# Kernel optimization log

Measured on AMD Instinct MI355X. Metric: run time of the kernel, lower is better.

Reference implementation:

```python
import jax, jax.numpy as jnp
import numpy as np

EPS = 1e-5

def _face_normals(v, vi):
    # v: [B,V,3], vi: [F,3] -> [B,F,3]
    pts = v[:, vi]                                  # [B,F,3,3]
    n = jnp.cross(pts[:, :, 1] - pts[:, :, 0], pts[:, :, 2] - pts[:, :, 0])
    norm = jnp.linalg.norm(n, axis=-1, keepdims=True)
    return n / jnp.where(norm < EPS, 1.0, norm)

def _vert_normals(v, vi):
    fn = _face_normals(v, vi)                       # [B,F,3]
    fn_rep = jnp.repeat(fn, 3, axis=1)              # [B,3F,3] (one copy per face vertex)
    vn = jnp.zeros_like(v).at[:, vi.reshape(-1)].add(fn_rep)
    norm = jnp.linalg.norm(vn, axis=-1, keepdims=True)
    return vn / jnp.where(norm < EPS, 1.0, norm)

def _values_to_uv(values, index_image, bary_image):
    # values: [B,V,C]; index_image/bary_image: [U,U,3] -> [B,C,U,U]
    mask = jnp.all(index_image != -1, axis=-1)      # [U,U]
    idx = jnp.clip(index_image, 0, values.shape[1] - 1)
    vals = values[:, idx]                           # [B,U,U,3,C]
    uv = jnp.einsum('buvkc,uvk->bcuv', vals, bary_image.astype(values.dtype))
    return uv * mask[None, None].astype(values.dtype)

def _grid_sample_bilinear(img, gx, gy):
    # img: [B,C,H,W]; gx,gy: [N] in [-1,1]; align_corners=False, zero padding
    B, C, H, W = img.shape
    ix = ((gx + 1.0) * W - 1.0) * 0.5
    iy = ((gy + 1.0) * H - 1.0) * 0.5
    x0 = jnp.floor(ix); y0 = jnp.floor(iy)
    x1 = x0 + 1.0;      y1 = y0 + 1.0
    wx1 = ix - x0; wx0 = 1.0 - wx1
    wy1 = iy - y0; wy0 = 1.0 - wy1
    def gather(xi, yi):
        valid = (xi >= 0) & (xi < W) & (yi >= 0) & (yi < H)
        xc = jnp.clip(xi, 0, W - 1).astype(jnp.int32)
        yc = jnp.clip(yi, 0, H - 1).astype(jnp.int32)
        return img[:, :, yc, xc] * valid.astype(img.dtype)  # [B,C,N]
    return (gather(x0, y0) * (wx0 * wy0) + gather(x1, y0) * (wx1 * wy0)
          + gather(x0, y1) * (wx0 * wy1) + gather(x1, y1) * (wx1 * wy1))

def _sample_uv(values_uv, uv_coords, v2uv):
    g = uv_coords * 2.0 - 1.0                       # [T,2]
    vals = _grid_sample_bilinear(values_uv, g[:, 0], g[:, 1])  # [B,C,T]
    vals = jnp.transpose(vals, (0, 2, 1))           # [B,T,C]
    return vals[:, v2uv].mean(axis=2)               # [B,V,C]

def setup_inputs() -> dict:
    key = jax.random.key(0)
    ks = jax.random.split(key, 6)
    B, V, Fc, U, T, K = 8, 100000, 200000, 1024, 110000, 2
    verts = jax.random.normal(ks[0], (B, V, 3), jnp.float32)
    vi = jax.random.randint(ks[1], (Fc, 3), 0, V, dtype=jnp.int32)
    index_image = jax.random.randint(ks[2], (U, U, 3), 0, V, dtype=jnp.int32)
    bary_image = jax.random.uniform(ks[3], (U, U, 3), jnp.float32)
    vt = jax.random.uniform(ks[4], (T, 2), jnp.float32)
    v2uv = jax.random.randint(ks[5], (V, K), 0, T, dtype=jnp.int32)
    return {"verts": verts, "bary_image": bary_image, "vt": vt,
            "vi": vi, "index_image": index_image, "v2uv": v2uv}

def reference(verts, bary_image, vt, vi, index_image, v2uv):
    vn = _vert_normals(verts, vi)                   # [B,V,3]
    uv = _values_to_uv(vn, index_image, bary_image) # [B,3,U,U]
    return _sample_uv(uv, vt, v2uv)                 # [B,V,3]
```

## Files before the change

kernel.cpp:

```cpp
#include <hip/hip_runtime.h>

#define EPS 1e-5f

constexpr int B = 8;
constexpr int V = 100000;
constexpr int F = 200000;
constexpr int U = 1024;
constexpr int T = 110000;
constexpr int ELLCAP = 32;

constexpr int TRB = (V + 255) / 256;
constexpr int CZB = (V + 255) / 256;
constexpr int ELB = (3 * F + 255) / 256;
constexpr int FNB = (F * 8 + 255) / 256;
constexpr int CPB = (T + 255) / 256;

struct Corner { int i0, i1, i2; float w0, w1, w2; };

__global__ void k1_pre(const float* __restrict__ verts,
                       float4* __restrict__ vertsT,
                       int* __restrict__ cnt) {
    int blk = blockIdx.x;
    if (blk < TRB) {
        int v = blk * 256 + threadIdx.x;
        if (v >= V) return;
        float4 row[8];
#pragma unroll
        for (int b = 0; b < 8; ++b) {
            const float* p = verts + (size_t)b * V * 3 + (size_t)v * 3;
            row[b] = make_float4(p[0], p[1], p[2], 0.0f);
        }
        float4* dst = vertsT + (size_t)v * 8;
#pragma unroll
        for (int b = 0; b < 8; ++b) dst[b] = row[b];
    } else {
        int i = (blk - TRB) * 256 + threadIdx.x;
        if (i < V) cnt[i] = 0;
    }
}

__global__ void k2_fused(const int* __restrict__ vi,
                         int* __restrict__ cnt,
                         int* __restrict__ ell,
                         const float4* __restrict__ vertsT,
                         float4* __restrict__ fn,
                         const int* __restrict__ index_image,
                         const float* __restrict__ bary_image,
                         const float* __restrict__ vt,
                         Corner* __restrict__ corners) {
    int blk = blockIdx.x;

    if (blk < ELB) {
        int e = blk * 256 + threadIdx.x;
        if (e >= 3 * F) return;
        int v = vi[e];
        int pos = atomicAdd(&cnt[v], 1);
        if (pos < ELLCAP) ell[v * ELLCAP + pos] = e / 3;
        return;
    }

    if (blk < ELB + FNB) {
        int id = (blk - ELB) * 256 + threadIdx.x;
        if (id >= F * 8) return;
        int f = id >> 3;
        int b = id & 7;

        int i0 = vi[f * 3 + 0];
        int i1 = vi[f * 3 + 1];
        int i2 = vi[f * 3 + 2];

        float4 p0 = vertsT[(size_t)i0 * 8 + b];
        float4 p1 = vertsT[(size_t)i1 * 8 + b];
        float4 p2 = vertsT[(size_t)i2 * 8 + b];

        float e1x = p1.x - p0.x, e1y = p1.y - p0.y, e1z = p1.z - p0.z;
        float e2x = p2.x - p0.x, e2y = p2.y - p0.y, e2z = p2.z - p0.z;

        float nx = e1y * e2z - e1z * e2y;
        float ny = e1z * e2x - e1x * e2z;
        float nz = e1x * e2y - e1y * e2x;

        float norm = sqrtf(nx * nx + ny * ny + nz * nz);
        float inv = (norm < EPS) ? 1.0f : (1.0f / norm);
        fn[id] = make_float4(nx * inv, ny * inv, nz * inv, 0.0f);
        return;
    }

    int t = (blk - ELB - FNB) * 256 + threadIdx.x;
    if (t >= T) return;

    float gx = vt[t * 2 + 0];
    float gy = vt[t * 2 + 1];
    float ix = gx * (float)U - 0.5f;
    float iy = gy * (float)U - 0.5f;

    float x0f = floorf(ix);
    float y0f = floorf(iy);
    int x0 = (int)x0f;
    int y0 = (int)y0f;
    float wx1 = ix - x0f, wx0 = 1.0f - wx1;
    float wy1 = iy - y0f, wy0 = 1.0f - wy1;

#pragma unroll
    for (int c = 0; c < 4; ++c) {
        int cy = c >> 1, cx = c & 1;
        int y = y0 + cy;
        int x = x0 + cx;
        Corner cr;
        if (x >= 0 && x < U && y >= 0 && y < U) {
            float w = (cy ? wy1 : wy0) * (cx ? wx1 : wx0);
            int pix = y * U + x;
            int i0 = index_image[pix * 3 + 0];
            int i1 = index_image[pix * 3 + 1];
            int i2 = index_image[pix * 3 + 2];
            float m = (i0 != -1 && i1 != -1 && i2 != -1) ? 1.0f : 0.0f;
            float wm = w * m;
            cr.i0 = min(max(i0, 0), V - 1);
            cr.i1 = min(max(i1, 0), V - 1);
            cr.i2 = min(max(i2, 0), V - 1);
            cr.w0 = wm * bary_image[pix * 3 + 0];
            cr.w1 = wm * bary_image[pix * 3 + 1];
            cr.w2 = wm * bary_image[pix * 3 + 2];
        } else {
            cr.i0 = 0; cr.i1 = 0; cr.i2 = 0;
            cr.w0 = 0.0f; cr.w1 = 0.0f; cr.w2 = 0.0f;
        }
        corners[t * 4 + c] = cr;
    }
}

__global__ void gather_vn(const float4* __restrict__ fn,
                          const int* __restrict__ cnt,
                          const int* __restrict__ ell,
                          float4* __restrict__ vn) {
    int id = blockIdx.x * blockDim.x + threadIdx.x;
    if (id >= V * 8) return;
    int v = id >> 3;
    int b = id & 7;

    int deg = min(cnt[v], ELLCAP);
    const int* row = ell + (size_t)v * ELLCAP;

    float ax = 0.0f, ay = 0.0f, az = 0.0f;
    for (int j = 0; j < deg; ++j) {
        int f = row[j];
        float4 n = fn[(size_t)f * 8 + b];
        ax += n.x; ay += n.y; az += n.z;
    }

    float n = sqrtf(ax * ax + ay * ay + az * az);
    float inv = (n < EPS) ? 1.0f : (1.0f / n);
    vn[id] = make_float4(ax * inv, ay * inv, az * inv, 0.0f);
}

__global__ void sample_points(const float4* __restrict__ vn,
                              const Corner* __restrict__ corners,
                              float4* __restrict__ vals) {
    int id = blockIdx.x * blockDim.x + threadIdx.x;
    if (id >= T * 8) return;
    int t = id >> 3;
    int b = id & 7;

    float ax = 0.0f, ay = 0.0f, az = 0.0f;
#pragma unroll
    for (int c = 0; c < 4; ++c) {
        Corner cr = corners[t * 4 + c];
        float4 q0 = vn[(size_t)cr.i0 * 8 + b];
        float4 q1 = vn[(size_t)cr.i1 * 8 + b];
        float4 q2 = vn[(size_t)cr.i2 * 8 + b];
        ax += cr.w0 * q0.x + cr.w1 * q1.x + cr.w2 * q2.x;
        ay += cr.w0 * q0.y + cr.w1 * q1.y + cr.w2 * q2.y;
        az += cr.w0 * q0.z + cr.w1 * q1.z + cr.w2 * q2.z;
    }

    vals[id] = make_float4(ax, ay, az, 0.0f);
}

__global__ void gather_out(const float4* __restrict__ vals,
                           const int* __restrict__ v2uv,
                           float* __restrict__ out) {
    int id = blockIdx.x * blockDim.x + threadIdx.x;
    if (id >= V * 8) return;
    int v = id >> 3;
    int b = id & 7;

    int t0 = v2uv[v * 2 + 0];
    int t1 = v2uv[v * 2 + 1];
    float4 x = vals[(size_t)t0 * 8 + b];
    float4 y = vals[(size_t)t1 * 8 + b];

    float* o = out + (size_t)b * V * 3 + (size_t)v * 3;
    o[0] = 0.5f * (x.x + y.x);
    o[1] = 0.5f * (x.y + y.y);
    o[2] = 0.5f * (x.z + y.z);
}

extern "C" void kernel_launch(void* const* d_in, const int* in_sizes, int n_in,
                              void* d_out, int out_size, void* d_ws, size_t ws_size,
                              hipStream_t stream) {
    const float* verts   = (const float*)d_in[0];
    const float* bary    = (const float*)d_in[1];
    const float* vt      = (const float*)d_in[2];
    const int*   vi      = (const int*)d_in[3];
    const int*   idx_img = (const int*)d_in[4];
    const int*   v2uv    = (const int*)d_in[5];
    float* out = (float*)d_out;

    float4* vertsT  = (float4*)d_ws;
    float4* vn      = vertsT;
    float4* fn      = vertsT + (size_t)V * 8;
    float4* vals    = fn;
    int*    cnt     = (int*)(fn + (size_t)F * 8);
    int*    ell     = cnt + V;
    Corner* corners = (Corner*)(ell + (size_t)V * ELLCAP);

    const int BLK = 256;
    k1_pre<<<TRB + CZB, BLK, 0, stream>>>(verts, vertsT, cnt);
    k2_fused<<<ELB + FNB + CPB, BLK, 0, stream>>>(
        vi, cnt, ell, vertsT, fn, idx_img, bary, vt, corners);
    gather_vn<<<(V * 8 + BLK - 1) / BLK, BLK, 0, stream>>>(fn, cnt, ell, vn);
    sample_points<<<(T * 8 + BLK - 1) / BLK, BLK, 0, stream>>>(vn, corners, vals);
    gather_out<<<(V * 8 + BLK - 1) / BLK, BLK, 0, stream>>>(vals, v2uv, out);
}
```

Before: 208.0 us.

## Build per-block vertex adjacency in shared memory instead of global ELL atomics

Removes the global ELL adjacency build, which used atomics on a global count array plus a zeroing pass. Each 512-thread workgroup instead scans the full face-index array, collects the incident faces of its own 512 vertices into a shared-memory list with shared atomics, and then sums face normals for them. This drops the global atomics, the ELL table traffic and one zeroing pass. In exchange, every one of the ~196 workgroups rereads the entire index array (~2.4 MB), which greatly increases total read traffic. The per-vertex capacity also drops from 32 to 28.

```diff
diff --git a/kernel.cpp b/kernel.cpp
--- a/kernel.cpp
+++ b/kernel.cpp
@@ -7,41 +7,33 @@
 constexpr int F = 200000;
 constexpr int U = 1024;
 constexpr int T = 110000;
-constexpr int ELLCAP = 32;
 
 constexpr int TRB = (V + 255) / 256;
-constexpr int CZB = (V + 255) / 256;
-constexpr int ELB = (3 * F + 255) / 256;
 constexpr int FNB = (F * 8 + 255) / 256;
 constexpr int CPB = (T + 255) / 256;
 
+constexpr int VPW = 512;
+constexpr int KWG = (V + VPW - 1) / VPW;
+constexpr int CAP = 28;
+
 struct Corner { int i0, i1, i2; float w0, w1, w2; };
 
-__global__ void k1_pre(const float* __restrict__ verts,
-                       float4* __restrict__ vertsT,
-                       int* __restrict__ cnt) {
-    int blk = blockIdx.x;
-    if (blk < TRB) {
-        int v = blk * 256 + threadIdx.x;
-        if (v >= V) return;
-        float4 row[8];
-#pragma unroll
-        for (int b = 0; b < 8; ++b) {
-            const float* p = verts + (size_t)b * V * 3 + (size_t)v * 3;
-            row[b] = make_float4(p[0], p[1], p[2], 0.0f);
-        }
-        float4* dst = vertsT + (size_t)v * 8;
-#pragma unroll
-        for (int b = 0; b < 8; ++b) dst[b] = row[b];
-    } else {
-        int i = (blk - TRB) * 256 + threadIdx.x;
-        if (i < V) cnt[i] = 0;
-    }
+__global__ void k1_transpose(const float* __restrict__ verts,
+                             float4* __restrict__ vertsT) {
+    int v = blockIdx.x * blockDim.x + threadIdx.x;
+    if (v >= V) return;
+    float4 row[8];
+#pragma unroll
+    for (int b = 0; b < 8; ++b) {
+        const float* p = verts + (size_t)b * V * 3 + (size_t)v * 3;
+        row[b] = make_float4(p[0], p[1], p[2], 0.0f);
+    }
+    float4* dst = vertsT + (size_t)v * 8;
+#pragma unroll
+    for (int b = 0; b < 8; ++b) dst[b] = row[b];
 }
 
 __global__ void k2_fused(const int* __restrict__ vi,
-                         int* __restrict__ cnt,
-                         int* __restrict__ ell,
                          const float4* __restrict__ vertsT,
                          float4* __restrict__ fn,
                          const int* __restrict__ index_image,
@@ -50,17 +42,8 @@
                          Corner* __restrict__ corners) {
     int blk = blockIdx.x;
 
-    if (blk < ELB) {
-        int e = blk * 256 + threadIdx.x;
-        if (e >= 3 * F) return;
-        int v = vi[e];
-        int pos = atomicAdd(&cnt[v], 1);
-        if (pos < ELLCAP) ell[v * ELLCAP + pos] = e / 3;
-        return;
-    }
-
-    if (blk < ELB + FNB) {
-        int id = (blk - ELB) * 256 + threadIdx.x;
+    if (blk < FNB) {
+        int id = blk * 256 + threadIdx.x;
         if (id >= F * 8) return;
         int f = id >> 3;
         int b = id & 7;
@@ -86,7 +69,7 @@
         return;
     }
 
-    int t = (blk - ELB - FNB) * 256 + threadIdx.x;
+    int t = (blk - FNB) * 256 + threadIdx.x;
     if (t >= T) return;
 
     float gx = vt[t * 2 + 0];
@@ -129,28 +112,56 @@
     }
 }
 
-__global__ void gather_vn(const float4* __restrict__ fn,
-                          const int* __restrict__ cnt,
-                          const int* __restrict__ ell,
-                          float4* __restrict__ vn) {
-    int id = blockIdx.x * blockDim.x + threadIdx.x;
-    if (id >= V * 8) return;
-    int v = id >> 3;
-    int b = id & 7;
-
-    int deg = min(cnt[v], ELLCAP);
-    const int* row = ell + (size_t)v * ELLCAP;
-
-    float ax = 0.0f, ay = 0.0f, az = 0.0f;
-    for (int j = 0; j < deg; ++j) {
-        int f = row[j];
-        float4 n = fn[(size_t)f * 8 + b];
-        ax += n.x; ay += n.y; az += n.z;
-    }
-
-    float n = sqrtf(ax * ax + ay * ay + az * az);
-    float inv = (n < EPS) ? 1.0f : (1.0f / n);
-    vn[id] = make_float4(ax * inv, ay * inv, az * inv, 0.0f);
+__global__ __launch_bounds__(512) void adj_gather(
+        const int* __restrict__ vi,
+        const float4* __restrict__ fn,
+        float4* __restrict__ vn) {
+    __shared__ int s_row[VPW * CAP];
+    __shared__ int s_cnt[VPW];
+    int tid = threadIdx.x;
+    int v0 = blockIdx.x * VPW;
+
+    for (int i = tid; i < VPW; i += 512) s_cnt[i] = 0;
+    __syncthreads();
+
+    const int4* vi4 = (const int4*)vi;
+    const int n4 = (3 * F) / 4;
+    for (int m4 = tid; m4 < n4; m4 += 512) {
+        int4 e = vi4[m4];
+        int base = m4 * 4;
+        int vv[4] = {e.x, e.y, e.z, e.w};
+#pragma unroll
+        for (int j = 0; j < 4; ++j) {
+            unsigned d = (unsigned)(vv[j] - v0);
+            if (d < (unsigned)VPW) {
+                int pos = atomicAdd(&s_cnt[d], 1);
+                if (pos < CAP) {
+                    int face = (int)(__umulhi((unsigned)(base + j), 0xAAAAAAABu) >> 1);
+                    s_row[d * CAP + pos] = face;
+                }
+            }
+        }
+    }
+    __syncthreads();
+
+    for (int id = tid; id < VPW * 8; id += 512) {
+        int vl = id >> 3;
+        int b = id & 7;
+        int v = v0 + vl;
+        if (v >= V) continue;
+        int deg = min(s_cnt[vl], CAP);
+        const int* row = s_row + vl * CAP;
+
+        float ax = 0.0f, ay = 0.0f, az = 0.0f;
+        for (int j = 0; j < deg; ++j) {
+            int f = row[j];
+            float4 n = fn[(size_t)f * 8 + b];
+            ax += n.x; ay += n.y; az += n.z;
+        }
+        float nn = sqrtf(ax * ax + ay * ay + az * az);
+        float inv = (nn < EPS) ? 1.0f : (1.0f / nn);
+        vn[(size_t)v * 8 + b] = make_float4(ax * inv, ay * inv, az * inv, 0.0f);
+    }
 }
 
 __global__ void sample_points(const float4* __restrict__ vn,
@@ -210,15 +221,13 @@
     float4* vn      = vertsT;
     float4* fn      = vertsT + (size_t)V * 8;
     float4* vals    = fn;
-    int*    cnt     = (int*)(fn + (size_t)F * 8);
-    int*    ell     = cnt + V;
-    Corner* corners = (Corner*)(ell + (size_t)V * ELLCAP);
+    Corner* corners = (Corner*)(fn + (size_t)F * 8);
 
     const int BLK = 256;
-    k1_pre<<<TRB + CZB, BLK, 0, stream>>>(verts, vertsT, cnt);
-    k2_fused<<<ELB + FNB + CPB, BLK, 0, stream>>>(
-        vi, cnt, ell, vertsT, fn, idx_img, bary, vt, corners);
-    gather_vn<<<(V * 8 + BLK - 1) / BLK, BLK, 0, stream>>>(fn, cnt, ell, vn);
+    k1_transpose<<<TRB, BLK, 0, stream>>>(verts, vertsT);
+    k2_fused<<<FNB + CPB, BLK, 0, stream>>>(
+        vi, vertsT, fn, idx_img, bary, vt, corners);
+    adj_gather<<<KWG, 512, 0, stream>>>(vi, fn, vn);
     sample_points<<<(T * 8 + BLK - 1) / BLK, BLK, 0, stream>>>(vn, corners, vals);
     gather_out<<<(V * 8 + BLK - 1) / BLK, BLK, 0, stream>>>(vals, v2uv, out);
 }
```

Measured after the change: 284.4 us. 36.7% more time.

## Interleave ELL build with face-normal blocks and vectorize corner storage

Applied to the files above, without the earlier changes.

Rearranges the fused kernel's block mapping so that each group of 17 blocks holds one ELL-build block, fifteen face-normal blocks and one corner block. This mixes atomic-heavy and compute-bound work across the GPU instead of running them as separate phases of the grid. The ELL build now loads vi as int4 and each thread does four atomics. The 24-byte Corner struct becomes separate int4 and float4 arrays so loads and stores are aligned and vectorized. ELL capacity drops from 32 to 24, which shrinks the ELL buffer but silently drops faces for any vertex with more than 24 incident faces.

```diff
diff --git a/kernel.cpp b/kernel.cpp
--- a/kernel.cpp
+++ b/kernel.cpp
@@ -7,15 +7,17 @@
 constexpr int F = 200000;
 constexpr int U = 1024;
 constexpr int T = 110000;
-constexpr int ELLCAP = 32;
+constexpr int CAP = 24;
 
 constexpr int TRB = (V + 255) / 256;
 constexpr int CZB = (V + 255) / 256;
-constexpr int ELB = (3 * F + 255) / 256;
-constexpr int FNB = (F * 8 + 255) / 256;
-constexpr int CPB = (T + 255) / 256;
-
-struct Corner { int i0, i1, i2; float w0, w1, w2; };
+
+constexpr int N4   = (3 * F) / 4;
+constexpr int ELLB = (N4 + 255) / 256;
+constexpr int FNB  = (F * 8 + 255) / 256;
+constexpr int CPB  = (T + 255) / 256;
+constexpr int PERIODS = ELLB;
+constexpr int K2N = PERIODS * 17;
 
 __global__ void k1_pre(const float* __restrict__ verts,
                        float4* __restrict__ vertsT,
@@ -47,20 +49,31 @@
                          const int* __restrict__ index_image,
                          const float* __restrict__ bary_image,
                          const float* __restrict__ vt,
-                         Corner* __restrict__ corners) {
-    int blk = blockIdx.x;
-
-    if (blk < ELB) {
-        int e = blk * 256 + threadIdx.x;
-        if (e >= 3 * F) return;
-        int v = vi[e];
-        int pos = atomicAdd(&cnt[v], 1);
-        if (pos < ELLCAP) ell[v * ELLCAP + pos] = e / 3;
+                         int4* __restrict__ cI,
+                         float4* __restrict__ cW) {
+    int p = blockIdx.x / 17;
+    int s = blockIdx.x % 17;
+
+    if (s == 0) {
+        int m4 = p * 256 + threadIdx.x;
+        if (m4 >= N4) return;
+        const int4* vi4 = (const int4*)vi;
+        int4 e = vi4[m4];
+        int base = m4 * 4;
+        int vv[4] = {e.x, e.y, e.z, e.w};
+#pragma unroll
+        for (int j = 0; j < 4; ++j) {
+            int v = vv[j];
+            int pos = atomicAdd(&cnt[v], 1);
+            if (pos < CAP) ell[v * CAP + pos] = (base + j) / 3;
+        }
         return;
     }
 
-    if (blk < ELB + FNB) {
-        int id = (blk - ELB) * 256 + threadIdx.x;
+    if (s <= 15) {
+        int bid = p * 15 + (s - 1);
+        if (bid >= FNB) return;
+        int id = bid * 256 + threadIdx.x;
         if (id >= F * 8) return;
         int f = id >> 3;
         int b = id & 7;
@@ -86,7 +99,8 @@
         return;
     }
 
-    int t = (blk - ELB - FNB) * 256 + threadIdx.x;
+    if (p >= CPB) return;
+    int t = p * 256 + threadIdx.x;
     if (t >= T) return;
 
     float gx = vt[t * 2 + 0];
@@ -106,7 +120,8 @@
         int cy = c >> 1, cx = c & 1;
         int y = y0 + cy;
         int x = x0 + cx;
-        Corner cr;
+        int4 ci = make_int4(0, 0, 0, 0);
+        float4 cw = make_float4(0.0f, 0.0f, 0.0f, 0.0f);
         if (x >= 0 && x < U && y >= 0 && y < U) {
             float w = (cy ? wy1 : wy0) * (cx ? wx1 : wx0);
             int pix = y * U + x;
@@ -115,17 +130,15 @@
             int i2 = index_image[pix * 3 + 2];
             float m = (i0 != -1 && i1 != -1 && i2 != -1) ? 1.0f : 0.0f;
             float wm = w * m;
-            cr.i0 = min(max(i0, 0), V - 1);
-            cr.i1 = min(max(i1, 0), V - 1);
-            cr.i2 = min(max(i2, 0), V - 1);
-            cr.w0 = wm * bary_image[pix * 3 + 0];
-            cr.w1 = wm * bary_image[pix * 3 + 1];
-            cr.w2 = wm * bary_image[pix * 3 + 2];
-        } else {
-            cr.i0 = 0; cr.i1 = 0; cr.i2 = 0;
-            cr.w0 = 0.0f; cr.w1 = 0.0f; cr.w2 = 0.0f;
+            ci.x = min(max(i0, 0), V - 1);
+            ci.y = min(max(i1, 0), V - 1);
+            ci.z = min(max(i2, 0), V - 1);
+            cw.x = wm * bary_image[pix * 3 + 0];
+            cw.y = wm * bary_image[pix * 3 + 1];
+            cw.z = wm * bary_image[pix * 3 + 2];
         }
-        corners[t * 4 + c] = cr;
+        cI[t * 4 + c] = ci;
+        cW[t * 4 + c] = cw;
     }
 }
 
@@ -138,8 +151,8 @@
     int v = id >> 3;
     int b = id & 7;
 
-    int deg = min(cnt[v], ELLCAP);
-    const int* row = ell + (size_t)v * ELLCAP;
+    int deg = min(cnt[v], CAP);
+    const int* row = ell + (size_t)v * CAP;
 
     float ax = 0.0f, ay = 0.0f, az = 0.0f;
     for (int j = 0; j < deg; ++j) {
@@ -154,7 +167,8 @@
 }
 
 __global__ void sample_points(const float4* __restrict__ vn,
-                              const Corner* __restrict__ corners,
+                              const int4* __restrict__ cI,
+                              const float4* __restrict__ cW,
                               float4* __restrict__ vals) {
     int id = blockIdx.x * blockDim.x + threadIdx.x;
     if (id >= T * 8) return;
@@ -164,13 +178,14 @@
     float ax = 0.0f, ay = 0.0f, az = 0.0f;
 #pragma unroll
     for (int c = 0; c < 4; ++c) {
-        Corner cr = corners[t * 4 + c];
-        float4 q0 = vn[(size_t)cr.i0 * 8 + b];
-        float4 q1 = vn[(size_t)cr.i1 * 8 + b];
-        float4 q2 = vn[(size_t)cr.i2 * 8 + b];
-        ax += cr.w0 * q0.x + cr.w1 * q1.x + cr.w2 * q2.x;
-        ay += cr.w0 * q0.y + cr.w1 * q1.y + cr.w2 * q2.y;
-        az += cr.w0 * q0.z + cr.w1 * q1.z + cr.w2 * q2.z;
+        int4 ci = cI[t * 4 + c];
+        float4 cw = cW[t * 4 + c];
+        float4 q0 = vn[(size_t)ci.x * 8 + b];
+        float4 q1 = vn[(size_t)ci.y * 8 + b];
+        float4 q2 = vn[(size_t)ci.z * 8 + b];
+        ax += cw.x * q0.x + cw.y * q1.x + cw.z * q2.x;
+        ay += cw.x * q0.y + cw.y * q1.y + cw.z * q2.y;
+        az += cw.x * q0.z + cw.y * q1.z + cw.z * q2.z;
     }
 
     vals[id] = make_float4(ax, ay, az, 0.0f);
@@ -206,19 +221,20 @@
     const int*   v2uv    = (const int*)d_in[5];
     float* out = (float*)d_out;
 
-    float4* vertsT  = (float4*)d_ws;
-    float4* vn      = vertsT;
-    float4* fn      = vertsT + (size_t)V * 8;
-    float4* vals    = fn;
-    int*    cnt     = (int*)(fn + (size_t)F * 8);
-    int*    ell     = cnt + V;
-    Corner* corners = (Corner*)(ell + (size_t)V * ELLCAP);
+    float4* vertsT = (float4*)d_ws;
+    float4* vn     = vertsT;
+    float4* fn     = vertsT + (size_t)V * 8;
+    float4* vals   = fn;
+    int4*   cI     = (int4*)(fn + (size_t)F * 8);
+    float4* cW     = (float4*)(cI + (size_t)T * 4);
+    int*    cnt    = (int*)(cW + (size_t)T * 4);
+    int*    ell    = cnt + V;
 
     const int BLK = 256;
     k1_pre<<<TRB + CZB, BLK, 0, stream>>>(verts, vertsT, cnt);
-    k2_fused<<<ELB + FNB + CPB, BLK, 0, stream>>>(
-        vi, cnt, ell, vertsT, fn, idx_img, bary, vt, corners);
+    k2_fused<<<K2N, BLK, 0, stream>>>(
+        vi, cnt, ell, vertsT, fn, idx_img, bary, vt, cI, cW);
     gather_vn<<<(V * 8 + BLK - 1) / BLK, BLK, 0, stream>>>(fn, cnt, ell, vn);
-    sample_points<<<(T * 8 + BLK - 1) / BLK, BLK, 0, stream>>>(vn, corners, vals);
+    sample_points<<<(T * 8 + BLK - 1) / BLK, BLK, 0, stream>>>(vn, cI, cW, vals);
     gather_out<<<(V * 8 + BLK - 1) / BLK, BLK, 0, stream>>>(vals, v2uv, out);
 }
```

New measurement: 195.9 us. 1.06x faster.
